# Optimization experiments

Measured on AMD Instinct MI355X. Metric: run time of the kernel, lower is better.

Reference implementation:

```python
import jax, jax.numpy as jnp
import numpy as np

N = 50000        # num nodes
E = 1600000      # num edges (before self loops)
F_IN = 128
F_OUT = 64
SLOPE = 0.2      # PyG GATConv default negative_slope


def setup_inputs() -> dict:
    key = jax.random.key(0)
    k0, k1, k2, k3, k4, k5 = jax.random.split(key, 6)
    x = jax.random.normal(k0, (N, F_IN), dtype=jnp.float32)
    # GATConv params (heads=1): linear weight, attention vectors, bias
    W = jax.random.normal(k1, (F_IN, F_OUT), dtype=jnp.float32) * (1.0 / np.sqrt(F_IN))
    a_src = jax.random.normal(k2, (F_OUT,), dtype=jnp.float32) * (1.0 / np.sqrt(F_OUT))
    a_dst = jax.random.normal(k3, (F_OUT,), dtype=jnp.float32) * (1.0 / np.sqrt(F_OUT))
    bias = jax.random.normal(k4, (F_OUT,), dtype=jnp.float32) * 0.01
    edge_index = jax.random.randint(k5, (2, E), 0, N, dtype=jnp.int32)
    return {"x": x, "W": W, "a_src": a_src, "a_dst": a_dst, "bias": bias,
            "edge_index": edge_index}


def reference(x, W, a_src, a_dst, bias, edge_index):
    # Linear transform: [N, F_OUT]
    xp = x @ W
    # add self loops (PyG GATConv default add_self_loops=True)
    loop = jnp.arange(N, dtype=edge_index.dtype)
    src = jnp.concatenate([edge_index[0], loop])  # source j of edge j->i
    dst = jnp.concatenate([edge_index[1], loop])  # target i
    # per-node attention logits, gathered per edge
    alpha_s = xp @ a_src  # [N]
    alpha_d = xp @ a_dst  # [N]
    e = alpha_s[src] + alpha_d[dst]               # [E+N]
    e = jnp.where(e > 0, e, SLOPE * e)            # leaky_relu(0.2)
    # segment softmax over edges grouped by destination node
    emax = jax.ops.segment_max(e, dst, num_segments=N)  # every node has a self loop
    w = jnp.exp(e - emax[dst])
    denom = jax.ops.segment_sum(w, dst, num_segments=N)
    alpha = w / denom[dst]                        # [E+N]
    # scatter-aggregate weighted source features
    out = jax.ops.segment_sum(alpha[:, None] * xp[src], dst, num_segments=N)
    out = out + bias
    # F.relu then unsqueeze(dim=0) and cat with empty -> [1, N, F_OUT]
    return jax.nn.relu(out)[None, :, :]
```

## Files before the change

kernel.cpp:

```cpp
#include <hip/hip_runtime.h>
#include <hip/hip_fp16.h>
#include <math.h>

#define N_NODES 50000
#define N_EDGES 1600000
#define ET (N_EDGES + N_NODES)
#define F_OUT 64
#define F_IN 128
#define SLOPE 0.2f
#define BSHIFT 7
#define BNODES 128
#define NBUCK ((N_NODES + BNODES - 1) >> BSHIFT)
#define CAP 4736
#define EPB 4096
#define PBLOCKS ((ET + EPB - 1) / EPB)

typedef _Float16 half8 __attribute__((ext_vector_type(8)));
typedef _Float16 half4 __attribute__((ext_vector_type(4)));
typedef float f32x4 __attribute__((ext_vector_type(4)));

__global__ __launch_bounds__(256) void gemm_kernel(const float4* __restrict__ x4,
                                                   const float4* __restrict__ W4,
                                                   const float* __restrict__ a_src,
                                                   const float* __restrict__ a_dst,
                                                   _Float16* __restrict__ xph,
                                                   float* __restrict__ alpha_s,
                                                   float* __restrict__ alpha_d,
                                                   int* __restrict__ bcur) {
    __shared__ _Float16 xs[64][136];
    __shared__ float    Wsh[F_IN * F_OUT];
    int t = threadIdx.x;
    if (blockIdx.x == 0)
        for (int i = t; i < NBUCK; i += 256) bcur[i] = 0;
    int wave = t >> 6, lane = t & 63;
    int g = lane >> 4, c16 = lane & 15;

#pragma unroll
    for (int i = 0; i < 8; ++i)
        ((float4*)Wsh)[t + i * 256] = W4[t + i * 256];
    size_t rbase = (size_t)blockIdx.x * 64;
#pragma unroll
    for (int i = 0; i < 8; ++i) {
        int idx = t + i * 256;
        int row = idx >> 5, c4 = idx & 31;
        size_t gr = rbase + row;
        if (gr >= N_NODES) gr = N_NODES - 1;
        float4 v = x4[gr * (F_IN / 4) + c4];
        half4 hv = { (_Float16)v.x, (_Float16)v.y, (_Float16)v.z, (_Float16)v.w };
        *(half4*)&xs[row][c4 * 4] = hv;
    }
    __syncthreads();

    half8 bw[4][4];
#pragma unroll
    for (int nt = 0; nt < 4; ++nt)
#pragma unroll
        for (int kt = 0; kt < 4; ++kt) {
            int col = nt * 16 + c16;
            int k0 = kt * 32 + g * 8;
#pragma unroll
            for (int e = 0; e < 8; ++e)
                bw[nt][kt][e] = (_Float16)Wsh[(k0 + e) * F_OUT + col];
        }

    int r0 = wave * 16;
    half8 af[4];
#pragma unroll
    for (int kt = 0; kt < 4; ++kt)
        af[kt] = *(const half8*)&xs[r0 + c16][kt * 32 + g * 8];

    f32x4 acc[4];
#pragma unroll
    for (int nt = 0; nt < 4; ++nt) {
        acc[nt] = (f32x4){0.f, 0.f, 0.f, 0.f};
#pragma unroll
        for (int kt = 0; kt < 4; ++kt)
            acc[nt] = __builtin_amdgcn_mfma_f32_16x16x32_f16(af[kt], bw[nt][kt], acc[nt], 0, 0, 0);
    }

    int growbase = (int)rbase + r0 + g * 4;
#pragma unroll
    for (int nt = 0; nt < 4; ++nt) {
#pragma unroll
        for (int r = 0; r < 4; ++r) {
            int row = growbase + r;
            if (row < N_NODES)
                xph[(size_t)row * F_OUT + nt * 16 + c16] = (_Float16)acc[nt][r];
        }
    }
    float asl[4], adl[4];
#pragma unroll
    for (int nt = 0; nt < 4; ++nt) {
        asl[nt] = a_src[nt * 16 + c16];
        adl[nt] = a_dst[nt * 16 + c16];
    }
#pragma unroll
    for (int r = 0; r < 4; ++r) {
        float ps = 0.f, pd = 0.f;
#pragma unroll
        for (int nt = 0; nt < 4; ++nt) {
            ps = fmaf(acc[nt][r], asl[nt], ps);
            pd = fmaf(acc[nt][r], adl[nt], pd);
        }
#pragma unroll
        for (int off = 1; off < 16; off <<= 1) {
            ps += __shfl_xor(ps, off);
            pd += __shfl_xor(pd, off);
        }
        int row = growbase + r;
        if (c16 == 0 && row < N_NODES) { alpha_s[row] = ps; alpha_d[row] = pd; }
    }
}

__global__ __launch_bounds__(256) void part_kernel(const int* __restrict__ ei,
                                                   int* __restrict__ bcur,
                                                   unsigned* __restrict__ rec) {
    __shared__ int lc[NBUCK];
    __shared__ int lbase[NBUCK];
    int t = threadIdx.x;
    for (int b = t; b < NBUCK; b += 256) lc[b] = 0;
    __syncthreads();
    int e0 = blockIdx.x * EPB;

    unsigned u[16]; short bk[16]; unsigned short rk[16];
#pragma unroll
    for (int k = 0; k < 4; ++k) {
        int e = e0 + k * 1024 + t * 4;
        int4 sv, dv;
        if (e + 3 < N_EDGES) {
            sv = *(const int4*)&ei[e];
            dv = *(const int4*)&ei[N_EDGES + e];
        } else {
            int* sp = (int*)&sv; int* dp = (int*)&dv;
#pragma unroll
            for (int j = 0; j < 4; ++j) {
                int ee = e + j;
                if (ee < N_EDGES)      { sp[j] = ei[ee]; dp[j] = ei[N_EDGES + ee]; }
                else if (ee < ET)      { sp[j] = dp[j] = ee - N_EDGES; }
                else                   { sp[j] = dp[j] = -1; }
            }
        }
        const int* sp = (const int*)&sv; const int* dp = (const int*)&dv;
#pragma unroll
        for (int j = 0; j < 4; ++j) {
            int i = k * 4 + j;
            int d = dp[j];
            if (d >= 0) {
                int b = d >> BSHIFT;
                bk[i] = (short)b;
                rk[i] = (unsigned short)atomicAdd(&lc[b], 1);
                u[i] = (unsigned)sp[j] | ((unsigned)d << 16);
            } else bk[i] = -1;
        }
    }
    __syncthreads();
    for (int b = t; b < NBUCK; b += 256)
        lbase[b] = lc[b] ? (b * CAP + atomicAdd(&bcur[b], lc[b])) : 0;
    __syncthreads();
#pragma unroll
    for (int i = 0; i < 16; ++i)
        if (bk[i] >= 0) rec[lbase[bk[i]] + rk[i]] = u[i];
}

__device__ __forceinline__ int block_incl_scan(int v, int t, int* wsum) {
    int lane = t & 63, wave = t >> 6;
#pragma unroll
    for (int off = 1; off < 64; off <<= 1) {
        int n = __shfl_up(v, off);
        if (lane >= off) v += n;
    }
    if (lane == 63) wsum[wave] = v;
    __syncthreads();
    int add = 0;
    for (int w = 0; w < wave; ++w) add += wsum[w];
    return v + add;
}

__global__ __launch_bounds__(512) void csrb_kernel(const unsigned* __restrict__ rec,
                                                   const int* __restrict__ bcur,
                                                   const float* __restrict__ as,
                                                   const float* __restrict__ ad,
                                                   int* __restrict__ offsets,
                                                   int* __restrict__ counts,
                                                   unsigned* __restrict__ wcsr) {
    __shared__ unsigned lrec[CAP];
    __shared__ int lcnt[BNODES], loff[BNODES], lcur[BNODES];
    __shared__ float adl[BNODES];
    __shared__ int wsum[8];
    int t = threadIdx.x;
    int b = blockIdx.x;
    int n0 = b << BSHIFT;
    int r0 = b * CAP;
    int cnt_b = bcur[b];
    if (t < BNODES) {
        lcnt[t] = 0; lcur[t] = 0;
        adl[t] = (n0 + t < N_NODES) ? ad[n0 + t] : 0.f;
    }
    for (int i = t; i < cnt_b; i += 512) lrec[i] = rec[r0 + i];
    __syncthreads();
    for (int i = t; i < cnt_b; i += 512)
        atomicAdd(&lcnt[(lrec[i] >> 16) & (BNODES - 1)], 1);
    __syncthreads();
    int v = (t < BNODES) ? lcnt[t] : 0;
    int incl = block_incl_scan(v, t, wsum);
    if (t < BNODES) {
        loff[t] = incl - v;
        if (n0 + t < N_NODES) { counts[n0 + t] = v; offsets[n0 + t] = r0 + incl - v; }
    }
    __syncthreads();
    for (int i = t; i < cnt_b; i += 512) {
        unsigned u = lrec[i];
        int dl = (u >> 16) & (BNODES - 1);
        int s = u & 0xFFFFu;
        float ev = as[s] + adl[dl];
        ev = ev > 0.f ? ev : SLOPE * ev;
        float w = __expf(ev);
        int pos = atomicAdd(&lcur[dl], 1);
        wcsr[r0 + loff[dl] + pos] =
            (unsigned)s | ((unsigned)__half_as_ushort(__float2half(w)) << 16);
    }
}

#define CONSUME(u_, h_)                                                        \
    {                                                                          \
        float w = __half2float(__ushort_as_half((unsigned short)((u_) >> 16)));\
        float2 f0 = __half22float2(__builtin_bit_cast(__half2, (h_).x));       \
        float2 f1 = __half22float2(__builtin_bit_cast(__half2, (h_).y));       \
        acc.x = fmaf(w, f0.x, acc.x);                                          \
        acc.y = fmaf(w, f0.y, acc.y);                                          \
        acc.z = fmaf(w, f1.x, acc.z);                                          \
        acc.w = fmaf(w, f1.y, acc.w);                                          \
        ws += w;                                                               \
    }

__global__ __launch_bounds__(256) void gather_kernel(const unsigned* __restrict__ wcsr,
                                                     const int* __restrict__ offsets,
                                                     const int* __restrict__ counts,
                                                     const __half* __restrict__ xp,
                                                     const float* __restrict__ bias,
                                                     float* __restrict__ out) {
    __shared__ unsigned stage[4][64];
    int wave = threadIdx.x >> 6, lane = threadIdx.x & 63;
    int d = blockIdx.x * 4 + wave;
    if (d >= N_NODES) return;
    int start = offsets[d], cnt = counts[d];
    int q = lane >> 4, f = lane & 15;
    const uint2* xp2 = (const uint2*)xp;
    float4 acc = make_float4(0.f, 0.f, 0.f, 0.f);
    float ws = 0.f;

    for (int jb = 0; jb < cnt; jb += 64) {
        int iters = min(cnt - jb, 64);
        unsigned rc = (lane < iters) ? wcsr[start + jb + lane] : 0u;
        stage[wave][lane] = rc;
        int m = (iters - q + 3) >> 2;
        int M4 = (m + 3) & ~3;
        unsigned u0 = stage[wave][q];
        unsigned u1 = stage[wave][q + 4];
        unsigned u2 = stage[wave][q + 8];
        unsigned u3 = stage[wave][q + 12];
        uint2 h0 = xp2[(u0 & 0xFFFFu) * 16 + f];
        uint2 h1 = xp2[(u1 & 0xFFFFu) * 16 + f];
        uint2 h2 = xp2[(u2 & 0xFFFFu) * 16 + f];
        uint2 h3 = xp2[(u3 & 0xFFFFu) * 16 + f];
        for (int i = 0; i < M4; i += 4) {
            CONSUME(u0, h0);
            if (i + 4 < M4) { u0 = stage[wave][q + (i + 4) * 4];
                              h0 = xp2[(u0 & 0xFFFFu) * 16 + f]; }
            CONSUME(u1, h1);
            if (i + 5 < M4) { u1 = stage[wave][q + (i + 5) * 4];
                              h1 = xp2[(u1 & 0xFFFFu) * 16 + f]; }
            CONSUME(u2, h2);
            if (i + 6 < M4) { u2 = stage[wave][q + (i + 6) * 4];
                              h2 = xp2[(u2 & 0xFFFFu) * 16 + f]; }
            CONSUME(u3, h3);
            if (i + 7 < M4) { u3 = stage[wave][q + (i + 7) * 4];
                              h3 = xp2[(u3 & 0xFFFFu) * 16 + f]; }
        }
    }
#pragma unroll
    for (int off = 16; off < 64; off <<= 1) {
        acc.x += __shfl_xor(acc.x, off);
        acc.y += __shfl_xor(acc.y, off);
        acc.z += __shfl_xor(acc.z, off);
        acc.w += __shfl_xor(acc.w, off);
        ws    += __shfl_xor(ws, off);
    }
    if (q == 0) {
        float inv = 1.f / ws;
        float4 bl = ((const float4*)bias)[f];
        float4 o;
        o.x = fmaf(acc.x, inv, bl.x);
        o.y = fmaf(acc.y, inv, bl.y);
        o.z = fmaf(acc.z, inv, bl.z);
        o.w = fmaf(acc.w, inv, bl.w);
        o.x = o.x > 0.f ? o.x : 0.f;
        o.y = o.y > 0.f ? o.y : 0.f;
        o.z = o.z > 0.f ? o.z : 0.f;
        o.w = o.w > 0.f ? o.w : 0.f;
        ((float4*)out)[(size_t)d * 16 + f] = o;
    }
}

extern "C" void kernel_launch(void* const* d_in, const int* in_sizes, int n_in,
                              void* d_out, int out_size, void* d_ws, size_t ws_size,
                              hipStream_t stream) {
    const float* x     = (const float*)d_in[0];
    const float* W     = (const float*)d_in[1];
    const float* a_src = (const float*)d_in[2];
    const float* a_dst = (const float*)d_in[3];
    const float* bias  = (const float*)d_in[4];
    const int*   ei    = (const int*)d_in[5];
    float* out = (float*)d_out;

    _Float16* xph   = (_Float16*)d_ws;
    float*  as      = (float*)(xph + (size_t)N_NODES * F_OUT);
    float*  ad      = as + N_NODES;
    int*    counts  = (int*)(ad + N_NODES);
    int*    offsets = counts + N_NODES;
    int*    bcur    = offsets + N_NODES;
    unsigned* rec   = (unsigned*)(bcur + NBUCK + 64);
    unsigned* wcsr  = rec + (size_t)NBUCK * CAP;

    gemm_kernel<<<(N_NODES + 63) / 64, 256, 0, stream>>>(
        (const float4*)x, (const float4*)W, a_src, a_dst, xph, as, ad, bcur);
    part_kernel<<<PBLOCKS, 256, 0, stream>>>(ei, bcur, rec);
    csrb_kernel<<<NBUCK, 512, 0, stream>>>(rec, bcur, as, ad, offsets, counts, wcsr);
    gather_kernel<<<(N_NODES + 3) / 4, 256, 0, stream>>>(wcsr, offsets, counts,
                                                         (const __half*)xph, bias, out);
}
```

Before: 85.84 us.

## Stage partition records in LDS, load W directly, deepen gather prefetch

The partition kernel now runs a block scan over bucket counts, writes records into a bucket-sorted shared buffer, and then copies them out with contiguous indices. This is meant to coalesce the scattered global writes. The GEMM kernel drops its shared-memory copy of W and has each lane read W directly from global memory into registers. The gather loop keeps 8 neighbor rows in flight instead of 4 to hide more latency. The costs are extra LDS use and syncs in partition, uncoalesced W reads in the GEMM, and more registers in the gather kernel.

```diff
diff --git a/kernel.cpp b/kernel.cpp
--- a/kernel.cpp
+++ b/kernel.cpp
@@ -20,7 +20,7 @@
 typedef float f32x4 __attribute__((ext_vector_type(4)));
 
 __global__ __launch_bounds__(256) void gemm_kernel(const float4* __restrict__ x4,
-                                                   const float4* __restrict__ W4,
+                                                   const float* __restrict__ W,
                                                    const float* __restrict__ a_src,
                                                    const float* __restrict__ a_dst,
                                                    _Float16* __restrict__ xph,
@@ -28,16 +28,12 @@
                                                    float* __restrict__ alpha_d,
                                                    int* __restrict__ bcur) {
     __shared__ _Float16 xs[64][136];
-    __shared__ float    Wsh[F_IN * F_OUT];
     int t = threadIdx.x;
     if (blockIdx.x == 0)
         for (int i = t; i < NBUCK; i += 256) bcur[i] = 0;
     int wave = t >> 6, lane = t & 63;
     int g = lane >> 4, c16 = lane & 15;
 
-#pragma unroll
-    for (int i = 0; i < 8; ++i)
-        ((float4*)Wsh)[t + i * 256] = W4[t + i * 256];
     size_t rbase = (size_t)blockIdx.x * 64;
 #pragma unroll
     for (int i = 0; i < 8; ++i) {
@@ -49,7 +45,6 @@
         half4 hv = { (_Float16)v.x, (_Float16)v.y, (_Float16)v.z, (_Float16)v.w };
         *(half4*)&xs[row][c4 * 4] = hv;
     }
-    __syncthreads();
 
     half8 bw[4][4];
 #pragma unroll
@@ -60,8 +55,9 @@
             int k0 = kt * 32 + g * 8;
 #pragma unroll
             for (int e = 0; e < 8; ++e)
-                bw[nt][kt][e] = (_Float16)Wsh[(k0 + e) * F_OUT + col];
-        }
+                bw[nt][kt][e] = (_Float16)W[(k0 + e) * F_OUT + col];
+        }
+    __syncthreads();
 
     int r0 = wave * 16;
     half8 af[4];
@@ -112,11 +108,29 @@
     }
 }
 
+__device__ __forceinline__ int block_incl_scan(int v, int t, int* wsum) {
+    int lane = t & 63, wave = t >> 6;
+#pragma unroll
+    for (int off = 1; off < 64; off <<= 1) {
+        int n = __shfl_up(v, off);
+        if (lane >= off) v += n;
+    }
+    if (lane == 63) wsum[wave] = v;
+    __syncthreads();
+    int add = 0;
+    for (int w = 0; w < wave; ++w) add += wsum[w];
+    return v + add;
+}
+
 __global__ __launch_bounds__(256) void part_kernel(const int* __restrict__ ei,
                                                    int* __restrict__ bcur,
                                                    unsigned* __restrict__ rec) {
     __shared__ int lc[NBUCK];
-    __shared__ int lbase[NBUCK];
+    __shared__ int lbl[NBUCK];
+    __shared__ int shift[NBUCK];
+    __shared__ unsigned lrec[EPB];
+    __shared__ int wsum[4];
+    __shared__ int tot1;
     int t = threadIdx.x;
     for (int b = t; b < NBUCK; b += 256) lc[b] = 0;
     __syncthreads();
@@ -154,15 +168,31 @@
         }
     }
     __syncthreads();
-    for (int b = t; b < NBUCK; b += 256)
-        lbase[b] = lc[b] ? (b * CAP + atomicAdd(&bcur[b], lc[b])) : 0;
-    __syncthreads();
+    int v0 = lc[t];
+    int incl0 = block_incl_scan(v0, t, wsum);
+    if (t == 255) tot1 = incl0;
+    lbl[t] = incl0 - v0;
+    __syncthreads();
+    int v1 = (t < NBUCK - 256) ? lc[256 + t] : 0;
+    int incl1 = block_incl_scan(v1, t, wsum);
+    if (t < NBUCK - 256) lbl[256 + t] = tot1 + incl1 - v1;
+    __syncthreads();
+    for (int b = t; b < NBUCK; b += 256) {
+        int c = lc[b];
+        if (c) shift[b] = b * CAP + atomicAdd(&bcur[b], c) - lbl[b];
+    }
 #pragma unroll
     for (int i = 0; i < 16; ++i)
-        if (bk[i] >= 0) rec[lbase[bk[i]] + rk[i]] = u[i];
-}
-
-__device__ __forceinline__ int block_incl_scan(int v, int t, int* wsum) {
+        if (bk[i] >= 0) lrec[lbl[bk[i]] + rk[i]] = u[i];
+    __syncthreads();
+    int total = lbl[NBUCK - 1] + lc[NBUCK - 1];
+    for (int i = t; i < total; i += 256) {
+        unsigned uu = lrec[i];
+        rec[shift[uu >> 23] + i] = uu;
+    }
+}
+
+__device__ __forceinline__ int block_incl_scan8(int v, int t, int* wsum) {
     int lane = t & 63, wave = t >> 6;
 #pragma unroll
     for (int off = 1; off < 64; off <<= 1) {
@@ -202,7 +232,7 @@
         atomicAdd(&lcnt[(lrec[i] >> 16) & (BNODES - 1)], 1);
     __syncthreads();
     int v = (t < BNODES) ? lcnt[t] : 0;
-    int incl = block_incl_scan(v, t, wsum);
+    int incl = block_incl_scan8(v, t, wsum);
     if (t < BNODES) {
         loff[t] = incl - v;
         if (n0 + t < N_NODES) { counts[n0 + t] = v; offsets[n0 + t] = r0 + incl - v; }
@@ -232,6 +262,10 @@
         acc.w = fmaf(w, f1.y, acc.w);                                          \
         ws += w;                                                               \
     }
+#define STEP(K, u_, h_)                                                        \
+    CONSUME(u_, h_);                                                           \
+    if (i + 8 + (K) < M8) { u_ = stage[wave][q + (i + 8 + (K)) * 4];           \
+                            h_ = xp2[((u_) & 0xFFFFu) * 16 + f]; }
 
 __global__ __launch_bounds__(256) void gather_kernel(const unsigned* __restrict__ wcsr,
                                                      const int* __restrict__ offsets,
@@ -254,28 +288,32 @@
         unsigned rc = (lane < iters) ? wcsr[start + jb + lane] : 0u;
         stage[wave][lane] = rc;
         int m = (iters - q + 3) >> 2;
-        int M4 = (m + 3) & ~3;
+        int M8 = (m + 7) & ~7;
         unsigned u0 = stage[wave][q];
         unsigned u1 = stage[wave][q + 4];
         unsigned u2 = stage[wave][q + 8];
         unsigned u3 = stage[wave][q + 12];
+        unsigned u4 = stage[wave][q + 16];
+        unsigned u5 = stage[wave][q + 20];
+        unsigned u6 = stage[wave][q + 24];
+        unsigned u7 = stage[wave][q + 28];
         uint2 h0 = xp2[(u0 & 0xFFFFu) * 16 + f];
         uint2 h1 = xp2[(u1 & 0xFFFFu) * 16 + f];
         uint2 h2 = xp2[(u2 & 0xFFFFu) * 16 + f];
         uint2 h3 = xp2[(u3 & 0xFFFFu) * 16 + f];
-        for (int i = 0; i < M4; i += 4) {
-            CONSUME(u0, h0);
-            if (i + 4 < M4) { u0 = stage[wave][q + (i + 4) * 4];
-                              h0 = xp2[(u0 & 0xFFFFu) * 16 + f]; }
-            CONSUME(u1, h1);
-            if (i + 5 < M4) { u1 = stage[wave][q + (i + 5) * 4];
-                              h1 = xp2[(u1 & 0xFFFFu) * 16 + f]; }
-            CONSUME(u2, h2);
-            if (i + 6 < M4) { u2 = stage[wave][q + (i + 6) * 4];
-                              h2 = xp2[(u2 & 0xFFFFu) * 16 + f]; }
-            CONSUME(u3, h3);
-            if (i + 7 < M4) { u3 = stage[wave][q + (i + 7) * 4];
-                              h3 = xp2[(u3 & 0xFFFFu) * 16 + f]; }
+        uint2 h4 = xp2[(u4 & 0xFFFFu) * 16 + f];
+        uint2 h5 = xp2[(u5 & 0xFFFFu) * 16 + f];
+        uint2 h6 = xp2[(u6 & 0xFFFFu) * 16 + f];
+        uint2 h7 = xp2[(u7 & 0xFFFFu) * 16 + f];
+        for (int i = 0; i < M8; i += 8) {
+            STEP(0, u0, h0);
+            STEP(1, u1, h1);
+            STEP(2, u2, h2);
+            STEP(3, u3, h3);
+            STEP(4, u4, h4);
+            STEP(5, u5, h5);
+            STEP(6, u6, h6);
+            STEP(7, u7, h7);
         }
     }
 #pragma unroll
@@ -323,7 +361,7 @@
     unsigned* wcsr  = rec + (size_t)NBUCK * CAP;
 
     gemm_kernel<<<(N_NODES + 63) / 64, 256, 0, stream>>>(
-        (const float4*)x, (const float4*)W, a_src, a_dst, xph, as, ad, bcur);
+        (const float4*)x, W, a_src, a_dst, xph, as, ad, bcur);
     part_kernel<<<PBLOCKS, 256, 0, stream>>>(ei, bcur, rec);
     csrb_kernel<<<NBUCK, 512, 0, stream>>>(rec, bcur, as, ad, offsets, counts, wcsr);
     gather_kernel<<<(N_NODES + 3) / 4, 256, 0, stream>>>(wcsr, offsets, counts,
```

After: 87.15 us. About the same (+1.5%).
